# Optimization experiments

Measured on AMD Instinct MI355X. Metric: run time of the kernel, lower is better.

Reference implementation:

```python
import jax, jax.numpy as jnp
import numpy as np

N = 100000   # nodes
E = 500000   # edges per relation
D = 128      # in_dim == out_dim
R = 3        # relations
NEG_SLOPE = 0.2  # DGL GATConv default


def setup_inputs() -> dict:
    key = jax.random.key(0)
    ks = jax.random.split(key, 7)
    x = jax.random.normal(ks[0], (N, D), jnp.float32)
    src = jax.random.randint(ks[1], (R, E), 0, N, jnp.int32)
    dst = jax.random.randint(ks[2], (R, E), 0, N, jnp.int32)
    W = jax.random.normal(ks[3], (R, D, D), jnp.float32) * 0.05
    attn_l = jax.random.normal(ks[4], (R, D), jnp.float32) * 0.05
    attn_r = jax.random.normal(ks[5], (R, D), jnp.float32) * 0.05
    bias = jnp.zeros((R, D), jnp.float32)
    return {"x": x, "src": src, "dst": dst, "W": W,
            "attn_l": attn_l, "attn_r": attn_r, "bias": bias}


def _gat_rel(x, src, dst, W, al, ar, b):
    # GATConv, num_heads=1: project, per-edge attention, segment softmax over dst
    feat = x @ W.T                                   # [N, D]
    el = (feat * al).sum(-1)                         # [N]
    er = (feat * ar).sum(-1)                         # [N]
    e = jax.nn.leaky_relu(el[src] + er[dst], NEG_SLOPE)   # [E]
    m = jax.ops.segment_max(e, dst, num_segments=N)       # stable softmax max per dst
    ex = jnp.exp(e - m[dst])
    s = jax.ops.segment_sum(ex, dst, num_segments=N)
    alpha = ex / s[dst]                                    # edge softmax weights
    out = jax.ops.segment_sum(alpha[:, None] * feat[src], dst, num_segments=N)
    return out + b                                         # GATConv bias


def reference(x, src, dst, W, attn_l, attn_r, bias):
    # HeteroGraphConv(aggregate='mean') over relations, then squeeze(head dim)
    outs = [_gat_rel(x, src[r], dst[r], W[r], attn_l[r], attn_r[r], bias[r])
            for r in range(R)]
    return jnp.mean(jnp.stack(outs, axis=0), axis=0)
```

## Files before the change

kernel.cpp:

```cpp
#include <hip/hip_runtime.h>
#include <hip/hip_bf16.h>

#define NN 100000
#define DD 128
#define RR 3
#define EE 500000
#define CAP 44
#define BK 196
#define ECAP 8192
#define SELR 50176
#define GEMM_NB 782
#define PART_NB 733

using bf16 = __hip_bfloat16;
typedef __attribute__((ext_vector_type(8))) short short8;
typedef __attribute__((ext_vector_type(4))) float f32x4;

__device__ __forceinline__ unsigned short f2bf(float f) {
  unsigned int u = __float_as_uint(f);
  return (unsigned short)((u + 0x7fffu + ((u >> 16) & 1u)) >> 16);
}
__device__ __forceinline__ float blo(unsigned int u) { return __uint_as_float(u << 16); }
__device__ __forceinline__ float bhi(unsigned int u) { return __uint_as_float(u & 0xffff0000u); }

__device__ __forceinline__ void ld_lds16(const void* g, void* l) {
  __builtin_amdgcn_global_load_lds((const __attribute__((address_space(1))) unsigned int*)g,
                                   (__attribute__((address_space(3))) unsigned int*)l, 16, 0, 0);
}

__global__ __launch_bounds__(256) void k_pre(
    const float* __restrict__ W, const float* __restrict__ bias,
    short* __restrict__ Wb, float* __restrict__ bm, int* __restrict__ gcur)
{
  int idx = blockIdx.x * 256 + threadIdx.x;
  float4 v = ((const float4*)W)[idx];
  short4 s;
  s.x = (short)f2bf(v.x); s.y = (short)f2bf(v.y);
  s.z = (short)f2bf(v.z); s.w = (short)f2bf(v.w);
  ((short4*)Wb)[idx] = s;
  if (blockIdx.x == 0 && threadIdx.x < DD) {
    int t = threadIdx.x;
    bm[t] = (bias[t] + bias[DD + t] + bias[2 * DD + t]) * (1.f / 3.f);
  }
  if (blockIdx.x == 1 && threadIdx.x < BK) gcur[threadIdx.x] = 0;
}

__device__ __forceinline__ void gemm_body(
    char* smem, int bid,
    const float* __restrict__ x, const short* __restrict__ Wb,
    const float* __restrict__ attn_l, const float* __restrict__ attn_r,
    short* __restrict__ feat, float* __restrict__ el, float* __restrict__ er)
{
  const int t = threadIdx.x, lane = t & 63, wave = t >> 6;
  const int row0 = bid * 128;
  const int ml = lane & 15, q = lane >> 4;
  const int wr = wave >> 1, wc = wave & 1;

  {
    const int rbase = t >> 5, c4 = t & 31;
    const int chunk = c4 >> 1, half = c4 & 1;
    const int dst0 = ((chunk ^ (rbase & 7)) << 4) + (half << 3);
    const float4* x4 = (const float4*)x;
#pragma unroll 4
    for (int i = 0; i < 16; ++i) {
      int row = i * 8 + rbase;
      int grow = row0 + row; if (grow >= NN) grow = NN - 1;
      float4 v = x4[(size_t)grow * 32 + c4];
      unsigned int p0 = ((unsigned int)f2bf(v.y) << 16) | f2bf(v.x);
      unsigned int p1 = ((unsigned int)f2bf(v.w) << 16) | f2bf(v.z);
      *(uint2*)(smem + row * 256 + dst0) = make_uint2(p0, p1);
    }
  }

  int mbase[4], nbase[4];
#pragma unroll
  for (int i = 0; i < 4; ++i) {
    mbase[i] = (wr * 64 + i * 16 + ml) * 256;
    nbase[i] = 32768 + (wc * 64 + i * 16 + ml) * 256;
  }

  for (int rel = 0; rel < RR; ++rel) {
    if (rel) __syncthreads();
    {
      const int rloc = q & 3;
#pragma unroll
      for (int i = 0; i < 8; ++i) {
        int rowB = wave * 32 + i * 4 + rloc;
        int c = ml ^ (rowB & 7);
        const short* gp = Wb + (size_t)(rel * 128 + rowB) * 128 + c * 8;
        ld_lds16(gp, smem + 32768 + wave * 8192 + i * 1024);
      }
    }
    __syncthreads();

    f32x4 acc[4][4] = {};
#pragma unroll
    for (int kc = 0; kc < 4; ++kc) {
      const int sw = ((kc * 4 + q) ^ (ml & 7)) << 4;
      short8 av[4], bv[4];
#pragma unroll
      for (int i = 0; i < 4; ++i) av[i] = *(const short8*)(smem + mbase[i] + sw);
#pragma unroll
      for (int i = 0; i < 4; ++i) bv[i] = *(const short8*)(smem + nbase[i] + sw);
#pragma unroll
      for (int mi = 0; mi < 4; ++mi)
#pragma unroll
        for (int ni = 0; ni < 4; ++ni)
          acc[mi][ni] = __builtin_amdgcn_mfma_f32_16x16x32_bf16(av[mi], bv[ni], acc[mi][ni], 0, 0, 0);
    }

    float pel[4][4], per_[4][4];
    {
      float alv[4], arv[4];
#pragma unroll
      for (int ni = 0; ni < 4; ++ni) {
        int c = rel * DD + wc * 64 + ni * 16 + ml;
        alv[ni] = attn_l[c]; arv[ni] = attn_r[c];
      }
#pragma unroll
      for (int mi = 0; mi < 4; ++mi)
#pragma unroll
        for (int reg = 0; reg < 4; ++reg) {
          float se = 0.f, sr = 0.f;
#pragma unroll
          for (int ni = 0; ni < 4; ++ni) {
            se = fmaf(acc[mi][ni][reg], alv[ni], se);
            sr = fmaf(acc[mi][ni][reg], arv[ni], sr);
          }
          pel[mi][reg] = se; per_[mi][reg] = sr;
        }
#pragma unroll
      for (int msk = 1; msk < 16; msk <<= 1)
#pragma unroll
        for (int mi = 0; mi < 4; ++mi)
#pragma unroll
          for (int reg = 0; reg < 4; ++reg) {
            pel[mi][reg]  += __shfl_xor(pel[mi][reg], msk);
            per_[mi][reg] += __shfl_xor(per_[mi][reg], msk);
          }
    }

    char* fb = (char*)feat + (size_t)rel * NN * 256;
#pragma unroll
    for (int p = 0; p < 2; ++p) {
      __syncthreads();
      if (p == 0 && ml == 0) {
#pragma unroll
        for (int mi = 0; mi < 4; ++mi)
#pragma unroll
          for (int reg = 0; reg < 4; ++reg) {
            int row = wr * 64 + mi * 16 + q * 4 + reg;
            *(float*)(smem + SELR + row * 16 + wc * 4)     = pel[mi][reg];
            *(float*)(smem + SELR + row * 16 + 8 + wc * 4) = per_[mi][reg];
          }
      }
      if (wr == p) {
#pragma unroll
        for (int mi = 0; mi < 4; ++mi)
#pragma unroll
          for (int ni = 0; ni < 4; ++ni) {
            f32x4 v = acc[mi][ni];
#pragma unroll
            for (int reg = 0; reg < 4; ++reg) {
              int rl = mi * 16 + q * 4 + reg;
              *(short*)(smem + 32768 + rl * 272 + wc * 128 + ni * 32 + ml * 2) = (short)f2bf(v[reg]);
            }
          }
      }
      __syncthreads();
      if (p == 0 && t < 128 && row0 + t < NN) {
        float4 v = *(const float4*)(smem + SELR + t * 16);
        el[rel * NN + row0 + t] = v.x + v.y;
        er[rel * NN + row0 + t] = v.z + v.w;
      }
#pragma unroll
      for (int o = 0; o < 4; ++o) {
        int rl = o * 16 + (t >> 4);
        int coloff = (t & 15) * 16;
        int grow = row0 + p * 64 + rl;
        if (grow < NN) {
          int4 v = *(const int4*)(smem + 32768 + rl * 272 + coloff);
          *(int4*)(fb + (size_t)grow * 256 + coloff) = v;
        }
      }
    }
  }
}

__device__ __forceinline__ void part_body(
    char* smem, int vb,
    const int* __restrict__ src, const int* __restrict__ dst,
    int* __restrict__ gcur, int* __restrict__ ebuf)
{
  int* lh = (int*)smem;
  const int t = threadIdx.x;
  for (int b = t; b < BK; b += 256) lh[b] = 0;
  __syncthreads();

  int eb[8], ebk[8];
  const int base = vb * 2048 + t;
#pragma unroll
  for (int k = 0; k < 8; ++k) {
    int i = base + k * 256;
    ebk[k] = -1;
    if (i < RR * EE) {
      int d = __builtin_nontemporal_load(&dst[i]);
      int s = __builtin_nontemporal_load(&src[i]);
      int r = i >= 2 * EE ? 2 : (i >= EE ? 1 : 0);
      ebk[k] = d >> 9;
      eb[k] = ((d & 511) << 19) | (r << 17) | s;
      atomicAdd(&lh[ebk[k]], 1);
    }
  }
  __syncthreads();
  if (t < BK) {
    int v = lh[t];
    lh[t] = v ? atomicAdd(&gcur[t], v) : 0;
  }
  __syncthreads();
#pragma unroll
  for (int k = 0; k < 8; ++k) {
    if (ebk[k] >= 0) {
      int pos = atomicAdd(&lh[ebk[k]], 1);
      if (pos < ECAP) ebuf[ebk[k] * ECAP + pos] = eb[k];
    }
  }
}

__global__ __launch_bounds__(256, 2) void k_fused(
    const float* __restrict__ x, const short* __restrict__ Wb,
    const float* __restrict__ attn_l, const float* __restrict__ attn_r,
    short* __restrict__ feat, float* __restrict__ el, float* __restrict__ er,
    const int* __restrict__ src, const int* __restrict__ dst,
    int* __restrict__ gcur, int* __restrict__ ebuf)
{
  __shared__ __align__(16) char smem[65536];
  if (blockIdx.x < GEMM_NB) {
    gemm_body(smem, blockIdx.x, x, Wb, attn_l, attn_r, feat, el, er);
  } else {
    part_body(smem, blockIdx.x - GEMM_NB, src, dst, gcur, ebuf);
  }
}

__global__ __launch_bounds__(256) void k_build(
    const int* __restrict__ gcur, const int* __restrict__ ebuf,
    int* __restrict__ counts, int* __restrict__ payload)
{
  __shared__ int lcnt[512];
  const int b = blockIdx.x, t = threadIdx.x;
  lcnt[t] = 0; lcnt[t + 256] = 0;
  __syncthreads();
  int cnt = gcur[b]; if (cnt > ECAP) cnt = ECAP;
  const int n0 = b << 9;
  for (int i = t; i < cnt; i += 256) {
    int ent = ebuf[b * ECAP + i];
    int dlow = ent >> 19;
    int pos = atomicAdd(&lcnt[dlow], 1);
    if (pos < CAP)
      payload[(size_t)(n0 + dlow) * CAP + pos] = ((ent >> 17) & 3) * NN + (ent & 0x1FFFF);
  }
  __syncthreads();
  if (n0 + t < NN)       counts[n0 + t] = lcnt[t];
  if (n0 + t + 256 < NN) counts[n0 + t + 256] = lcnt[t + 256];
}

__global__ __launch_bounds__(256) void k_gather(
    const int* __restrict__ counts, const int* __restrict__ payload,
    const float* __restrict__ el, const float* __restrict__ er,
    const short* __restrict__ feat, const float* __restrict__ bm,
    float* __restrict__ out)
{
  const int lane = threadIdx.x & 63;
  const int hw = lane >> 4, m = lane & 15;
  const int n = blockIdx.x * 4 + (threadIdx.x >> 6);
  int deg = counts[n];
  deg = deg > CAP ? CAP : deg;
  const float er0 = er[n], er1 = er[NN + n], er2 = er[2 * NN + n];
  const bool act = lane < deg;
  int pl = act ? payload[(size_t)n * CAP + lane] : 0;
  int r = pl >= 2 * NN ? 2 : (pl >= NN ? 1 : 0);
  float ex = 0.f;
  if (act) {
    float e = el[pl] + (r == 0 ? er0 : (r == 1 ? er1 : er2));
    e = e >= 0.f ? e : 0.2f * e;
    ex = __expf(e);
  }
  float v0 = (act && r == 0) ? ex : 0.f;
  float v1 = (act && r == 1) ? ex : 0.f;
  float v2 = (act && r == 2) ? ex : 0.f;
#pragma unroll
  for (int msk = 1; msk < 64; msk <<= 1) {
    v0 += __shfl_xor(v0, msk);
    v1 += __shfl_xor(v1, msk);
    v2 += __shfl_xor(v2, msk);
  }
  float i0 = v0 > 0.f ? 1.f / v0 : 0.f;
  float i1 = v1 > 0.f ? 1.f / v1 : 0.f;
  float i2 = v2 > 0.f ? 1.f / v2 : 0.f;
  float w = ex * (r == 0 ? i0 : (r == 1 ? i1 : i2));

  float a8[8] = {0.f, 0.f, 0.f, 0.f, 0.f, 0.f, 0.f, 0.f};
  const unsigned short* fs = (const unsigned short*)feat;
  for (int e = 0; e < deg; e += 8) {
#pragma unroll
    for (int g = 0; g < 2; ++g) {
      int idx = e + g * 4 + hw;
      float we = __shfl(w, idx);
      int pe = __shfl(pl, idx);
      uint4 u = *(const uint4*)(fs + (size_t)pe * DD + m * 8);
      a8[0] = fmaf(we, blo(u.x), a8[0]); a8[1] = fmaf(we, bhi(u.x), a8[1]);
      a8[2] = fmaf(we, blo(u.y), a8[2]); a8[3] = fmaf(we, bhi(u.y), a8[3]);
      a8[4] = fmaf(we, blo(u.z), a8[4]); a8[5] = fmaf(we, bhi(u.z), a8[5]);
      a8[6] = fmaf(we, blo(u.w), a8[6]); a8[7] = fmaf(we, bhi(u.w), a8[7]);
    }
  }
#pragma unroll
  for (int k = 0; k < 8; ++k) {
    a8[k] += __shfl_xor(a8[k], 16);
    a8[k] += __shfl_xor(a8[k], 32);
  }
  if (hw == 0) {
    const int j = m * 8;
    float4 b0 = *(const float4*)(bm + j);
    float4 b1 = *(const float4*)(bm + j + 4);
    float4 o0, o1;
    o0.x = a8[0] * (1.f / 3.f) + b0.x; o0.y = a8[1] * (1.f / 3.f) + b0.y;
    o0.z = a8[2] * (1.f / 3.f) + b0.z; o0.w = a8[3] * (1.f / 3.f) + b0.w;
    o1.x = a8[4] * (1.f / 3.f) + b1.x; o1.y = a8[5] * (1.f / 3.f) + b1.y;
    o1.z = a8[6] * (1.f / 3.f) + b1.z; o1.w = a8[7] * (1.f / 3.f) + b1.w;
    float* op = out + (size_t)n * DD + j;
    *(float4*)op = o0;
    *(float4*)(op + 4) = o1;
  }
}

extern "C" void kernel_launch(void* const* d_in, const int* in_sizes, int n_in,
                              void* d_out, int out_size, void* d_ws, size_t ws_size,
                              hipStream_t stream)
{
  const float* x    = (const float*)d_in[0];
  const int*   src  = (const int*)d_in[1];
  const int*   dst  = (const int*)d_in[2];
  const float* W    = (const float*)d_in[3];
  const float* al   = (const float*)d_in[4];
  const float* ar   = (const float*)d_in[5];
  const float* bias = (const float*)d_in[6];
  float* out = (float*)d_out;

  char* p = (char*)d_ws;
  short* feat    = (short*)p; p += (size_t)RR * NN * DD * 2;
  int*   payload = (int*)p;   p += (size_t)NN * CAP * 4;
  int*   ebuf    = (int*)p;   p += (size_t)BK * ECAP * 4;
  float* el      = (float*)p; p += (size_t)RR * NN * 4;
  float* er      = (float*)p; p += (size_t)RR * NN * 4;
  short* Wb      = (short*)p; p += (size_t)RR * DD * DD * 2;
  float* bm      = (float*)p; p += (size_t)DD * 4;
  int*   counts  = (int*)p;   p += (size_t)NN * 4;
  int*   gcur    = (int*)p;   p += (size_t)BK * 4;

  k_pre<<<48, 256, 0, stream>>>(W, bias, Wb, bm, gcur);
  k_fused<<<GEMM_NB + PART_NB, 256, 0, stream>>>(x, Wb, al, ar, feat, el, er,
                                                 src, dst, gcur, ebuf);
  k_build<<<BK, 256, 0, stream>>>(gcur, ebuf, counts, payload);
  k_gather<<<NN / 4, 256, 0, stream>>>(counts, payload, el, er, feat, bm, out);
}
```

Measured before the change: 246.6 us.

## Replace two-pass bucketed edge partition with direct global atomics; pipeline gather loads

The edge partitioning no longer bins edges into coarse buckets and rebuilds per-node lists in a separate kernel. Each edge now does a global atomicAdd on its destination counter and writes its payload slot directly, and the counters are zeroed in the prep kernel. This removes one kernel launch and the round trip through the intermediate buffer, at the cost of roughly 1.5M scattered global atomics. The gather loop is also restructured to fetch 16 edges per step with software prefetch of the next group, to overlap the feature loads with the FMAs.

```diff
diff --git a/kernel.cpp b/kernel.cpp
--- a/kernel.cpp
+++ b/kernel.cpp
@@ -6,8 +6,6 @@
 #define RR 3
 #define EE 500000
 #define CAP 44
-#define BK 196
-#define ECAP 8192
 #define SELR 50176
 #define GEMM_NB 782
 #define PART_NB 733
@@ -30,7 +28,7 @@
 
 __global__ __launch_bounds__(256) void k_pre(
     const float* __restrict__ W, const float* __restrict__ bias,
-    short* __restrict__ Wb, float* __restrict__ bm, int* __restrict__ gcur)
+    short* __restrict__ Wb, float* __restrict__ bm, int* __restrict__ counts)
 {
   int idx = blockIdx.x * 256 + threadIdx.x;
   float4 v = ((const float4*)W)[idx];
@@ -42,7 +40,8 @@
     int t = threadIdx.x;
     bm[t] = (bias[t] + bias[DD + t] + bias[2 * DD + t]) * (1.f / 3.f);
   }
-  if (blockIdx.x == 1 && threadIdx.x < BK) gcur[threadIdx.x] = 0;
+  int4 z4 = make_int4(0, 0, 0, 0);
+  for (int z = idx; z < NN / 4; z += 48 * 256) ((int4*)counts)[z] = z4;
 }
 
 __device__ __forceinline__ void gemm_body(
@@ -188,41 +187,21 @@
 }
 
 __device__ __forceinline__ void part_body(
-    char* smem, int vb,
-    const int* __restrict__ src, const int* __restrict__ dst,
-    int* __restrict__ gcur, int* __restrict__ ebuf)
-{
-  int* lh = (int*)smem;
+    int vb, const int* __restrict__ src, const int* __restrict__ dst,
+    int* __restrict__ counts, int* __restrict__ payload)
+{
   const int t = threadIdx.x;
-  for (int b = t; b < BK; b += 256) lh[b] = 0;
-  __syncthreads();
-
-  int eb[8], ebk[8];
   const int base = vb * 2048 + t;
 #pragma unroll
   for (int k = 0; k < 8; ++k) {
     int i = base + k * 256;
-    ebk[k] = -1;
     if (i < RR * EE) {
       int d = __builtin_nontemporal_load(&dst[i]);
       int s = __builtin_nontemporal_load(&src[i]);
       int r = i >= 2 * EE ? 2 : (i >= EE ? 1 : 0);
-      ebk[k] = d >> 9;
-      eb[k] = ((d & 511) << 19) | (r << 17) | s;
-      atomicAdd(&lh[ebk[k]], 1);
-    }
-  }
-  __syncthreads();
-  if (t < BK) {
-    int v = lh[t];
-    lh[t] = v ? atomicAdd(&gcur[t], v) : 0;
-  }
-  __syncthreads();
-#pragma unroll
-  for (int k = 0; k < 8; ++k) {
-    if (ebk[k] >= 0) {
-      int pos = atomicAdd(&lh[ebk[k]], 1);
-      if (pos < ECAP) ebuf[ebk[k] * ECAP + pos] = eb[k];
+      int pos = atomicAdd(&counts[d], 1);
+      if (pos < CAP)
+        payload[(size_t)d * CAP + pos] = r * NN + s;
     }
   }
 }
@@ -232,36 +211,14 @@
     const float* __restrict__ attn_l, const float* __restrict__ attn_r,
     short* __restrict__ feat, float* __restrict__ el, float* __restrict__ er,
     const int* __restrict__ src, const int* __restrict__ dst,
-    int* __restrict__ gcur, int* __restrict__ ebuf)
+    int* __restrict__ counts, int* __restrict__ payload)
 {
   __shared__ __align__(16) char smem[65536];
   if (blockIdx.x < GEMM_NB) {
     gemm_body(smem, blockIdx.x, x, Wb, attn_l, attn_r, feat, el, er);
   } else {
-    part_body(smem, blockIdx.x - GEMM_NB, src, dst, gcur, ebuf);
-  }
-}
-
-__global__ __launch_bounds__(256) void k_build(
-    const int* __restrict__ gcur, const int* __restrict__ ebuf,
-    int* __restrict__ counts, int* __restrict__ payload)
-{
-  __shared__ int lcnt[512];
-  const int b = blockIdx.x, t = threadIdx.x;
-  lcnt[t] = 0; lcnt[t + 256] = 0;
-  __syncthreads();
-  int cnt = gcur[b]; if (cnt > ECAP) cnt = ECAP;
-  const int n0 = b << 9;
-  for (int i = t; i < cnt; i += 256) {
-    int ent = ebuf[b * ECAP + i];
-    int dlow = ent >> 19;
-    int pos = atomicAdd(&lcnt[dlow], 1);
-    if (pos < CAP)
-      payload[(size_t)(n0 + dlow) * CAP + pos] = ((ent >> 17) & 3) * NN + (ent & 0x1FFFF);
-  }
-  __syncthreads();
-  if (n0 + t < NN)       counts[n0 + t] = lcnt[t];
-  if (n0 + t + 256 < NN) counts[n0 + t + 256] = lcnt[t + 256];
+    part_body(blockIdx.x - GEMM_NB, src, dst, counts, payload);
+  }
 }
 
 __global__ __launch_bounds__(256) void k_gather(
@@ -301,19 +258,46 @@
 
   float a8[8] = {0.f, 0.f, 0.f, 0.f, 0.f, 0.f, 0.f, 0.f};
   const unsigned short* fs = (const unsigned short*)feat;
-  for (int e = 0; e < deg; e += 8) {
-#pragma unroll
-    for (int g = 0; g < 2; ++g) {
-      int idx = e + g * 4 + hw;
-      float we = __shfl(w, idx);
-      int pe = __shfl(pl, idx);
-      uint4 u = *(const uint4*)(fs + (size_t)pe * DD + m * 8);
-      a8[0] = fmaf(we, blo(u.x), a8[0]); a8[1] = fmaf(we, bhi(u.x), a8[1]);
-      a8[2] = fmaf(we, blo(u.y), a8[2]); a8[3] = fmaf(we, bhi(u.y), a8[3]);
-      a8[4] = fmaf(we, blo(u.z), a8[4]); a8[5] = fmaf(we, bhi(u.z), a8[5]);
-      a8[6] = fmaf(we, blo(u.w), a8[6]); a8[7] = fmaf(we, bhi(u.w), a8[7]);
-    }
-  }
+
+#define FETCH16(E, W0, W1, W2, W3, U0, U1, U2, U3)                        \
+  do {                                                                    \
+    int i0_ = (E) + hw, i1_ = (E) + 4 + hw, i2_ = (E) + 8 + hw,           \
+        i3_ = (E) + 12 + hw;                                              \
+    W0 = __shfl(w, i0_); W1 = __shfl(w, i1_);                             \
+    W2 = __shfl(w, i2_); W3 = __shfl(w, i3_);                             \
+    int p0_ = __shfl(pl, i0_), p1_ = __shfl(pl, i1_),                     \
+        p2_ = __shfl(pl, i2_), p3_ = __shfl(pl, i3_);                     \
+    U0 = *(const uint4*)(fs + (size_t)p0_ * DD + m * 8);                  \
+    U1 = *(const uint4*)(fs + (size_t)p1_ * DD + m * 8);                  \
+    U2 = *(const uint4*)(fs + (size_t)p2_ * DD + m * 8);                  \
+    U3 = *(const uint4*)(fs + (size_t)p3_ * DD + m * 8);                  \
+  } while (0)
+
+#define FMA8(WE, U)                                                       \
+  do {                                                                    \
+    a8[0] = fmaf(WE, blo(U.x), a8[0]); a8[1] = fmaf(WE, bhi(U.x), a8[1]); \
+    a8[2] = fmaf(WE, blo(U.y), a8[2]); a8[3] = fmaf(WE, bhi(U.y), a8[3]); \
+    a8[4] = fmaf(WE, blo(U.z), a8[4]); a8[5] = fmaf(WE, bhi(U.z), a8[5]); \
+    a8[6] = fmaf(WE, blo(U.w), a8[6]); a8[7] = fmaf(WE, bhi(U.w), a8[7]); \
+  } while (0)
+
+  if (deg > 0) {
+    float cw0, cw1, cw2, cw3;
+    uint4 cu0, cu1, cu2, cu3;
+    FETCH16(0, cw0, cw1, cw2, cw3, cu0, cu1, cu2, cu3);
+    for (int e = 16; e < deg; e += 16) {
+      float nw0, nw1, nw2, nw3;
+      uint4 nu0, nu1, nu2, nu3;
+      FETCH16(e, nw0, nw1, nw2, nw3, nu0, nu1, nu2, nu3);
+      FMA8(cw0, cu0); FMA8(cw1, cu1); FMA8(cw2, cu2); FMA8(cw3, cu3);
+      cw0 = nw0; cw1 = nw1; cw2 = nw2; cw3 = nw3;
+      cu0 = nu0; cu1 = nu1; cu2 = nu2; cu3 = nu3;
+    }
+    FMA8(cw0, cu0); FMA8(cw1, cu1); FMA8(cw2, cu2); FMA8(cw3, cu3);
+  }
+#undef FETCH16
+#undef FMA8
+
 #pragma unroll
   for (int k = 0; k < 8; ++k) {
     a8[k] += __shfl_xor(a8[k], 16);
@@ -350,17 +334,14 @@
   char* p = (char*)d_ws;
   short* feat    = (short*)p; p += (size_t)RR * NN * DD * 2;
   int*   payload = (int*)p;   p += (size_t)NN * CAP * 4;
-  int*   ebuf    = (int*)p;   p += (size_t)BK * ECAP * 4;
   float* el      = (float*)p; p += (size_t)RR * NN * 4;
   float* er      = (float*)p; p += (size_t)RR * NN * 4;
   short* Wb      = (short*)p; p += (size_t)RR * DD * DD * 2;
   float* bm      = (float*)p; p += (size_t)DD * 4;
   int*   counts  = (int*)p;   p += (size_t)NN * 4;
-  int*   gcur    = (int*)p;   p += (size_t)BK * 4;
-
-  k_pre<<<48, 256, 0, stream>>>(W, bias, Wb, bm, gcur);
+
+  k_pre<<<48, 256, 0, stream>>>(W, bias, Wb, bm, counts);
   k_fused<<<GEMM_NB + PART_NB, 256, 0, stream>>>(x, Wb, al, ar, feat, el, er,
-                                                 src, dst, gcur, ebuf);
-  k_build<<<BK, 256, 0, stream>>>(gcur, ebuf, counts, payload);
+                                                 src, dst, counts, payload);
   k_gather<<<NN / 4, 256, 0, stream>>>(counts, payload, el, er, feat, bm, out);
 }
```

Result: slower. 272.6 us (+10.6%).
